# Kernel tuning notes

Hardware: AMD Instinct MI355X
Metric: run time of the kernel (lower is better)

## Reference

```python
import jax, jax.numpy as jnp
import numpy as np

EMBED_DIM = 1024
NUM_HEADS = 16
HEAD_DIM = EMBED_DIM // NUM_HEADS
TOPK_INIT = 0.3  # learnable scalar in torch; k = int(S*sigmoid(topk)) is non-differentiable, so static here


def setup_inputs() -> dict:
    rng = jax.random.key(0)
    ks = jax.random.split(rng, 11)
    L, N, E = 2048, 2, EMBED_DIM
    S = 2048
    w = 1.0 / np.sqrt(E)
    return {
        "query": jax.random.normal(ks[0], (L, N, E), jnp.float32),
        "key": jax.random.normal(ks[1], (S, N, E), jnp.float32),
        "value": jax.random.normal(ks[2], (S, N, E), jnp.float32),
        "Wq": jax.random.normal(ks[3], (E, E), jnp.float32) * w,
        "bq": jax.random.normal(ks[4], (E,), jnp.float32) * 0.02,
        "Wk": jax.random.normal(ks[5], (E, E), jnp.float32) * w,
        "bk": jax.random.normal(ks[6], (E,), jnp.float32) * 0.02,
        "Wv": jax.random.normal(ks[7], (E, E), jnp.float32) * w,
        "bv": jax.random.normal(ks[8], (E,), jnp.float32) * 0.02,
        "Wo": jax.random.normal(ks[9], (E, E), jnp.float32) * w,
        "bo": jax.random.normal(ks[10], (E,), jnp.float32) * 0.02,
    }


def reference(query, key, value, Wq, bq, Wk, bk, Wv, bv, Wo, bo):
    L, N, E = query.shape
    S = key.shape[0]
    H, D = NUM_HEADS, HEAD_DIM

    # Linear projections (nn.Linear: y = x @ W.T + b), then [L/S,N,E] -> [N,L/S,H,D]
    q = (query @ Wq.T + bq).reshape(L, N, H, D).transpose(1, 0, 2, 3)
    k = (key @ Wk.T + bk).reshape(S, N, H, D).transpose(1, 0, 2, 3)
    v = (value @ Wv.T + bv).reshape(S, N, H, D).transpose(1, 0, 2, 3)

    # [N, L, H, S]
    scores = jnp.einsum('nlhd,nshd->nlhs', q, k) / np.sqrt(D).astype(np.float32)

    # per-query top-k sparsification; k is static (int() of sigmoid(param) in torch)
    k_sel = int(S * (1.0 / (1.0 + np.exp(-TOPK_INIT))))
    _, topk_idx = jax.lax.top_k(scores, k_sel)
    keep = jnp.put_along_axis(
        jnp.zeros(scores.shape, dtype=bool), topk_idx, True, axis=-1, inplace=False
    )
    scores = jnp.where(keep, scores, -jnp.inf)
    attn = jax.nn.softmax(scores, axis=-1)

    # [N, L, D, H] (note d-major, h-minor ordering matches torch's view(L,N,E))
    out = jnp.einsum('nlhs,nshd->nldh', attn, v)
    out = out.transpose(1, 0, 2, 3).reshape(L, N, E)
    return out @ Wo.T + bo
```

## Files before the change

### kernel.cpp

```cpp
#include <hip/hip_runtime.h>
#include <hip/hip_bf16.h>
#include <hip/hip_fp16.h>


#define KSEL 1176u
#define SROW 2048
#define HSTR 132

typedef __attribute__((ext_vector_type(8))) short bf16x8;
typedef __attribute__((ext_vector_type(8))) _Float16 f16x8;
typedef __attribute__((ext_vector_type(4))) float f32x4;
typedef unsigned short ushort_t;

union S8 { bf16x8 v; ushort_t u[8]; };
union H8 { f16x8 v; ushort_t u[8]; };

#define MFMA16(A, B, C)  __builtin_amdgcn_mfma_f32_16x16x32_bf16(A, B, C, 0, 0, 0)
#define MFMAH16(A, B, C) __builtin_amdgcn_mfma_f32_16x16x32_f16(A, B, C, 0, 0, 0)

__device__ __forceinline__ ushort_t f2bf(float x) {
  unsigned u = __float_as_uint(x);
  return (ushort_t)((u + 0x7FFFu + ((u >> 16) & 1u)) >> 16);
}
__device__ __forceinline__ float bf2f(ushort_t b) {
  return __uint_as_float(((unsigned)b) << 16);
}
__device__ __forceinline__ ushort_t f2h(float x) {
  return __half_as_ushort(__float2half(x));
}
__device__ __forceinline__ float h2f(ushort_t b) {
  return __half2float(__ushort_as_half(b));
}

__device__ __forceinline__ void cvt8(ushort_t* dst, float4 p, float4 q) {
  H8 t;
  t.u[0] = f2h(p.x); t.u[1] = f2h(p.y); t.u[2] = f2h(p.z); t.u[3] = f2h(p.w);
  t.u[4] = f2h(q.x); t.u[5] = f2h(q.y); t.u[6] = f2h(q.z); t.u[7] = f2h(q.w);
  *(f16x8*)dst = t.v;
}

__global__ __launch_bounds__(256) void presplit_w(
    const float* __restrict__ W0, const float* __restrict__ W1,
    const float* __restrict__ W2, const float* __restrict__ W3,
    ushort_t* __restrict__ Whi, ushort_t* __restrict__ Wlo) {
  const int m = blockIdx.y;
  const float* W = (m == 0) ? W0 : (m == 1) ? W1 : (m == 2) ? W2 : W3;
  const size_t off = ((size_t)blockIdx.x * 256 + threadIdx.x) * 8;
  const size_t base = (size_t)m * 1048576 + off;
  if (m == 3) {
    const int f = (int)(off >> 10);
    const int r = (int)(off & 1023);
    const int hcol = r >> 6, d0 = r & 63;
    S8 hi_, lo_;
#pragma unroll
    for (int j = 0; j < 8; j++) {
      float x = W[(size_t)f * 1024 + (size_t)(d0 + j) * 16 + hcol];
      ushort_t hb = f2bf(x);
      hi_.u[j] = hb;
      lo_.u[j] = f2bf(x - bf2f(hb));
    }
    *(bf16x8*)&Whi[base] = hi_.v;
    *(bf16x8*)&Wlo[base] = lo_.v;
  } else {
    float4 p = *(const float4*)&W[off];
    float4 q = *(const float4*)&W[off + 4];
    cvt8(&Whi[base], p, q);
  }
}

__global__ __launch_bounds__(256, 4) void proj_qkv(
    const float* __restrict__ Xq, const float* __restrict__ Xk,
    const float* __restrict__ Xv, const float* __restrict__ bq,
    const float* __restrict__ bk, const float* __restrict__ bv,
    const ushort_t* __restrict__ Whi, ushort_t* __restrict__ Qf,
    ushort_t* __restrict__ Kf, ushort_t* __restrict__ Vt) {
  __shared__ ushort_t Ah[64 * 72], Bh[64 * 72];
  const int z = blockIdx.z;
  const float* X = (z == 0) ? Xq : (z == 1) ? Xk : Xv;
  const float* bias = (z == 0) ? bq : (z == 1) ? bk : bv;
  const size_t zoff = (size_t)z * 1048576;

  const int tid = threadIdx.x;
  const int n0 = blockIdx.x * 64, m0 = blockIdx.y * 64;
  const int lane = tid & 63, wv = tid >> 6;
  const int lg = lane >> 4, lq = lane & 15;
  const int wr = wv >> 1, wc = wv & 1;
  const int sr = tid >> 2, c8 = (tid & 3) * 8;

  f32x4 acc[2][2] = {};

  const float* Xr = &X[(size_t)(m0 + sr) * 1024 + c8];
  const ushort_t* Bhg = Whi + zoff + (size_t)(n0 + sr) * 1024 + c8;

  float4 a0 = *(const float4*)&Xr[0],  a1 = *(const float4*)&Xr[4];
  float4 a2 = *(const float4*)&Xr[32], a3 = *(const float4*)&Xr[36];
  f16x8 pb0 = *(const f16x8*)&Bhg[0], pb1 = *(const f16x8*)&Bhg[32];

  for (int k0 = 0; k0 < 1024; k0 += 64) {
    __syncthreads();
    cvt8(&Ah[sr * 72 + c8], a0, a1);
    cvt8(&Ah[sr * 72 + c8 + 32], a2, a3);
    *(f16x8*)&Bh[sr * 72 + c8] = pb0;
    *(f16x8*)&Bh[sr * 72 + c8 + 32] = pb1;
    if (k0 + 64 < 1024) {
      const float* Xn = Xr + k0 + 64;
      a0 = *(const float4*)&Xn[0];  a1 = *(const float4*)&Xn[4];
      a2 = *(const float4*)&Xn[32]; a3 = *(const float4*)&Xn[36];
      pb0 = *(const f16x8*)&Bhg[k0 + 64];
      pb1 = *(const f16x8*)&Bhg[k0 + 96];
    }
    __syncthreads();
#pragma unroll
    for (int kh = 0; kh < 2; kh++) {
      const int ko = kh * 32 + lg * 8;
      f16x8 bh0 = *(const f16x8*)&Bh[(wc * 32 + lq) * 72 + ko];
      f16x8 bh1 = *(const f16x8*)&Bh[(wc * 32 + 16 + lq) * 72 + ko];
#pragma unroll
      for (int i = 0; i < 2; i++) {
        f16x8 ahv = *(const f16x8*)&Ah[(wr * 32 + i * 16 + lq) * 72 + ko];
        acc[i][0] = MFMAH16(ahv, bh0, acc[i][0]);
        acc[i][1] = MFMAH16(ahv, bh1, acc[i][1]);
      }
    }
  }

  ushort_t* dqk = (z == 0) ? Qf : Kf;
#pragma unroll
  for (int i = 0; i < 2; i++)
#pragma unroll
    for (int j = 0; j < 2; j++)
#pragma unroll
      for (int ri = 0; ri < 4; ri++) {
        int m = m0 + wr * 32 + i * 16 + 4 * lg + ri;
        int e = n0 + wc * 32 + j * 16 + lq;
        float v = acc[i][j][ri] + bias[e];
        int l = m >> 1, n = m & 1, hh = e >> 6, d = e & 63;
        if (z == 2) {
          Vt[((size_t)(n * 16 + hh) * 64 + d) * 2048 + l] = f2h(v);
        } else {
          float x = (z == 0) ? v * 0.125f : v;
          dqk[((size_t)(n * 16 + hh) * 2048 + l) * 64 + d] = f2h(x);
        }
      }
}

__global__ __launch_bounds__(256, 4) void proj_out(
    const ushort_t* __restrict__ AOhi, const ushort_t* __restrict__ AOlo,
    const ushort_t* __restrict__ Whi3, const ushort_t* __restrict__ Wlo3,
    const float* __restrict__ bias, float* __restrict__ out) {
  __shared__ ushort_t Ah[64 * 72], Al[64 * 72], Bh[64 * 72], Bl[64 * 72];
  const int tid = threadIdx.x;
  const int n0 = blockIdx.x * 64, m0 = blockIdx.y * 64;
  const int lane = tid & 63, wv = tid >> 6;
  const int lg = lane >> 4, lq = lane & 15;
  const int wr = wv >> 1, wc = wv & 1;
  const int sr = tid >> 2, c8 = (tid & 3) * 8;

  f32x4 acc[2][2] = {};

  const size_t abase = (size_t)(m0 + sr) * 64 + c8;
  const ushort_t* Bhg = Whi3 + (size_t)(n0 + sr) * 1024 + c8;
  const ushort_t* Blg = Wlo3 + (size_t)(n0 + sr) * 1024 + c8;

  bf16x8 pa0 = *(const bf16x8*)&AOhi[abase], pa1 = *(const bf16x8*)&AOhi[abase + 32];
  bf16x8 pc0 = *(const bf16x8*)&AOlo[abase], pc1 = *(const bf16x8*)&AOlo[abase + 32];
  bf16x8 pb0 = *(const bf16x8*)&Bhg[0], pb1 = *(const bf16x8*)&Bhg[32];
  bf16x8 pl0 = *(const bf16x8*)&Blg[0], pl1 = *(const bf16x8*)&Blg[32];

  for (int k0 = 0; k0 < 1024; k0 += 64) {
    __syncthreads();
    *(bf16x8*)&Ah[sr * 72 + c8] = pa0;  *(bf16x8*)&Ah[sr * 72 + c8 + 32] = pa1;
    *(bf16x8*)&Al[sr * 72 + c8] = pc0;  *(bf16x8*)&Al[sr * 72 + c8 + 32] = pc1;
    *(bf16x8*)&Bh[sr * 72 + c8] = pb0;  *(bf16x8*)&Bh[sr * 72 + c8 + 32] = pb1;
    *(bf16x8*)&Bl[sr * 72 + c8] = pl0;  *(bf16x8*)&Bl[sr * 72 + c8 + 32] = pl1;
    if (k0 + 64 < 1024) {
      const size_t an = abase + (size_t)((k0 >> 6) + 1) * 262144;
      pa0 = *(const bf16x8*)&AOhi[an]; pa1 = *(const bf16x8*)&AOhi[an + 32];
      pc0 = *(const bf16x8*)&AOlo[an]; pc1 = *(const bf16x8*)&AOlo[an + 32];
      pb0 = *(const bf16x8*)&Bhg[k0 + 64]; pb1 = *(const bf16x8*)&Bhg[k0 + 96];
      pl0 = *(const bf16x8*)&Blg[k0 + 64]; pl1 = *(const bf16x8*)&Blg[k0 + 96];
    }
    __syncthreads();
#pragma unroll
    for (int kh = 0; kh < 2; kh++) {
      const int ko = kh * 32 + lg * 8;
      bf16x8 bh0 = *(const bf16x8*)&Bh[(wc * 32 + lq) * 72 + ko];
      bf16x8 bh1 = *(const bf16x8*)&Bh[(wc * 32 + 16 + lq) * 72 + ko];
      bf16x8 bl0 = *(const bf16x8*)&Bl[(wc * 32 + lq) * 72 + ko];
      bf16x8 bl1 = *(const bf16x8*)&Bl[(wc * 32 + 16 + lq) * 72 + ko];
#pragma unroll
      for (int i = 0; i < 2; i++) {
        bf16x8 ahv = *(const bf16x8*)&Ah[(wr * 32 + i * 16 + lq) * 72 + ko];
        bf16x8 alv = *(const bf16x8*)&Al[(wr * 32 + i * 16 + lq) * 72 + ko];
        acc[i][0] = MFMA16(ahv, bh0, acc[i][0]);
        acc[i][0] = MFMA16(alv, bh0, acc[i][0]);
        acc[i][0] = MFMA16(ahv, bl0, acc[i][0]);
        acc[i][1] = MFMA16(ahv, bh1, acc[i][1]);
        acc[i][1] = MFMA16(alv, bh1, acc[i][1]);
        acc[i][1] = MFMA16(ahv, bl1, acc[i][1]);
      }
    }
  }

#pragma unroll
  for (int i = 0; i < 2; i++)
#pragma unroll
    for (int j = 0; j < 2; j++)
#pragma unroll
      for (int ri = 0; ri < 4; ri++) {
        int m = m0 + wr * 32 + i * 16 + 4 * lg + ri;
        int e = n0 + wc * 32 + j * 16 + lq;
        out[(size_t)m * 1024 + e] = acc[i][j][ri] + bias[e];
      }
}

template <bool RANKMAP>
__device__ __forceinline__ void scan_row(const unsigned* hrow, unsigned target,
                                         int lane, int* binOut, unsigned* remOut) {
  unsigned c0, c1, c2, c3;
  if (RANKMAP) {
    const bool neg = lane >= 32;
    const int ho = neg ? (lane << 1) : (62 - (lane << 1));
    uint2 hw = *(const uint2*)&hrow[ho];
    unsigned a0 = hw.x & 0xffffu, a1 = hw.x >> 16;
    unsigned a2 = hw.y & 0xffffu, a3 = hw.y >> 16;
    c0 = neg ? a0 : a3; c1 = neg ? a1 : a2;
    c2 = neg ? a2 : a1; c3 = neg ? a3 : a0;
  } else {
    uint2 hw = *(const uint2*)&hrow[lane << 1];
    c0 = hw.x & 0xffffu; c1 = hw.x >> 16;
    c2 = hw.y & 0xffffu; c3 = hw.y >> 16;
  }
  unsigned s4 = c0 + c1 + c2 + c3, incl = s4;
#pragma unroll
  for (int off = 1; off < 64; off <<= 1) {
    unsigned t = __shfl_up(incl, off);
    if (lane >= off) incl += t;
  }
  unsigned excl = incl - s4;
  bool found = (excl < target) && (target <= incl);
  int b = 0; unsigned rm = 1;
  if (found) {
    unsigned cum = excl;
    if (cum + c0 >= target) { b = (lane << 2); rm = target - cum; }
    else { cum += c0;
      if (cum + c1 >= target) { b = (lane << 2) + 1; rm = target - cum; }
      else { cum += c1;
        if (cum + c2 >= target) { b = (lane << 2) + 2; rm = target - cum; }
        else { cum += c2; b = (lane << 2) + 3; rm = target - cum; } } }
  }
  unsigned long long bal = __ballot(found);
  int src = (int)__builtin_ctzll(bal);
  *binOut = __shfl(b, src);
  *remOut = (unsigned)__shfl((int)rm, src);
}

#define KLOAD(F, gg)                                                   \
  do {                                                                 \
    _Pragma("unroll") for (int tt = 0; tt < 4; tt++) {                 \
      const int koff = ((gg) * 4 + tt) * 1024;                         \
      F[tt * 2 + 0] = *(const f16x8*)&kbase[koff];                     \
      F[tt * 2 + 1] = *(const f16x8*)&kbase[koff + 32];                \
    }                                                                  \
  } while (0)

#define KCOMP(F, gg)                                                          \
  do {                                                                        \
    _Pragma("unroll") for (int tt = 0; tt < 4; tt++) {                        \
      f32x4 acc_ = {0.f, 0.f, 0.f, 0.f};                                      \
      acc_ = MFMAH16(F[tt * 2 + 0], qf0, acc_);                               \
      acc_ = MFMAH16(F[tt * 2 + 1], qf1, acc_);                               \
      uint2 pw_;                                                              \
      pw_.x = (unsigned)f2h(acc_[0]) | ((unsigned)f2h(acc_[1]) << 16);        \
      pw_.y = (unsigned)f2h(acc_[2]) | ((unsigned)f2h(acc_[3]) << 16);        \
      atomicAdd(&histP[lq * HSTR + ((pw_.x >> 9) & 0x7Fu)],                   \
                1u << (((pw_.x >> 8) & 1u) << 4));                            \
      atomicAdd(&histP[lq * HSTR + (pw_.x >> 25)],                            \
                1u << (((pw_.x >> 24) & 1u) << 4));                           \
      atomicAdd(&histP[lq * HSTR + ((pw_.y >> 9) & 0x7Fu)],                   \
                1u << (((pw_.y >> 8) & 1u) << 4));                            \
      atomicAdd(&histP[lq * HSTR + (pw_.y >> 25)],                            \
                1u << (((pw_.y >> 24) & 1u) << 4));                           \
      const int st_ = (w * 16 + (gg) * 4 + tt) * 16;                          \
      *(uint2*)&scH[lq * SROW + ((st_ + 4 * lg) ^ xr8q)] = pw_;               \
    }                                                                         \
  } while (0)

__global__ __launch_bounds__(512, 2) void sparse_attn(
    const ushort_t* __restrict__ Qf, const ushort_t* __restrict__ Kfp,
    const ushort_t* __restrict__ Vt, ushort_t* __restrict__ AOhi,
    ushort_t* __restrict__ AOlo) {
  __shared__ ushort_t scH[16 * SROW];
  __shared__ unsigned histP[16 * HSTR];
  __shared__ float Obuf[16 * 68];
  __shared__ float dinvS[16];

  const int flat = blockIdx.x + 128 * (blockIdx.y + 16 * blockIdx.z);
  const int idx = (flat & 7) * 512 + (flat >> 3);
  const int lb = idx & 127, h = (idx >> 7) & 15, n = idx >> 11;

  const int tid = threadIdx.x;
  const int lane = tid & 63, w = tid >> 6;
  const int lg = lane >> 4, lq = lane & 15;
  const int xr8q = (lq & 7) << 3;
  const size_t nh = (size_t)(n * 16 + h);

  for (int i = tid; i < 16 * HSTR; i += 512) histP[i] = 0u;
  for (int i = tid; i < 16 * 68; i += 512) Obuf[i] = 0.f;

  const size_t qo = (nh * 2048 + (size_t)lb * 16 + lq) * 64 + lg * 8;
  const f16x8 qf0 = *(const f16x8*)&Qf[qo];
  const f16x8 qf1 = *(const f16x8*)&Qf[qo + 32];

  const ushort_t* Kf = Kfp + nh * 2048 * 64;
  const ushort_t* kbase = Kf + (size_t)(w * 256 + lq) * 64 + lg * 8;

  __syncthreads();

  {
    f16x8 fa[8], fb[8];
    KLOAD(fa, 0);
    for (int g = 0; g < 4; g += 2) {
      KLOAD(fb, g + 1);
      KCOMP(fa, g);
      if (g + 2 < 4) KLOAD(fa, g + 2);
      KCOMP(fb, g + 1);
    }
  }
  __syncthreads();

  for (int rr = 0; rr < 2; rr++) {
    const int r = w * 2 + rr;
    const int rb = r * SROW;
    const int xr = (r & 7) << 3;
    unsigned* hrow = &histP[r * HSTR];

    int b1r; unsigned rem;
    scan_row<true>(hrow, KSEL, lane, &b1r, &rem);
    const unsigned rb1 = (b1r < 128) ? (unsigned)(b1r ^ 0x7F) : (unsigned)b1r;
    const unsigned sxor = (rb1 & 0x80u) ? 0u : 0xFFu;

    uint4 rv0 = *(const uint4*)&scH[rb + ((0 * 512 + lane * 8) ^ xr)];
    uint4 rv1 = *(const uint4*)&scH[rb + ((1 * 512 + lane * 8) ^ xr)];
    uint4 rv2 = *(const uint4*)&scH[rb + ((2 * 512 + lane * 8) ^ xr)];
    uint4 rv3 = *(const uint4*)&scH[rb + ((3 * 512 + lane * 8) ^ xr)];

    *(uint2*)&hrow[lane << 1] = make_uint2(0u, 0u);
    __threadfence_block();
    auto refine1 = [&](unsigned wd) {
      if (((wd >> 8) & 0xFFu) == rb1) {
        unsigned sr_ = (wd & 0xFFu) ^ sxor;
        atomicAdd(&hrow[sr_ >> 1], 1u << ((sr_ & 1u) << 4));
      }
      if ((wd >> 24) == rb1) {
        unsigned sr_ = ((wd >> 16) & 0xFFu) ^ sxor;
        atomicAdd(&hrow[sr_ >> 1], 1u << ((sr_ & 1u) << 4));
      }
    };
    refine1(rv0.x); refine1(rv0.y); refine1(rv0.z); refine1(rv0.w);
    refine1(rv1.x); refine1(rv1.y); refine1(rv1.z); refine1(rv1.w);
    refine1(rv2.x); refine1(rv2.y); refine1(rv2.z); refine1(rv2.w);
    refine1(rv3.x); refine1(rv3.y); refine1(rv3.z); refine1(rv3.w);
    __threadfence_block();
    int b2r; unsigned rem2;
    scan_row<false>(hrow, rem, lane, &b2r, &rem2);
    const unsigned vbits = (rb1 << 8) | (((unsigned)b2r) ^ sxor);
    const float fV = h2f((ushort_t)vbits);

    float den = 0.f;
    auto exp2w = [&](unsigned wd) -> unsigned {
      float f0 = h2f((ushort_t)(wd & 0xffffu));
      float f1 = h2f((ushort_t)(wd >> 16));
      float e0 = (f0 >= fV) ? __expf(f0) : 0.f;
      float e1 = (f1 >= fV) ? __expf(f1) : 0.f;
      den += e0 + e1;
      return (unsigned)f2h(e0) | ((unsigned)f2h(e1) << 16);
    };
    uint4 ov;
    ov.x = exp2w(rv0.x); ov.y = exp2w(rv0.y); ov.z = exp2w(rv0.z); ov.w = exp2w(rv0.w);
    *(uint4*)&scH[rb + ((0 * 512 + lane * 8) ^ xr)] = ov;
    ov.x = exp2w(rv1.x); ov.y = exp2w(rv1.y); ov.z = exp2w(rv1.z); ov.w = exp2w(rv1.w);
    *(uint4*)&scH[rb + ((1 * 512 + lane * 8) ^ xr)] = ov;
    ov.x = exp2w(rv2.x); ov.y = exp2w(rv2.y); ov.z = exp2w(rv2.z); ov.w = exp2w(rv2.w);
    *(uint4*)&scH[rb + ((2 * 512 + lane * 8) ^ xr)] = ov;
    ov.x = exp2w(rv3.x); ov.y = exp2w(rv3.y); ov.z = exp2w(rv3.z); ov.w = exp2w(rv3.w);
    *(uint4*)&scH[rb + ((3 * 512 + lane * 8) ^ xr)] = ov;

#pragma unroll
    for (int off = 32; off > 0; off >>= 1) den += __shfl_xor(den, off);
    if (lane == 0) dinvS[r] = 1.0f / den;
  }
  __syncthreads();

  {
    const int db = w & 3, sh = w >> 2;
    const int sOff = sh * 1024;
    const ushort_t* Vb =
        Vt + (nh * 64 + (size_t)(db * 16 + lq)) * 2048 + sOff;
    const int xw = (lq & 7) << 3;
    const int arow = lq * SROW;
    f32x4 o0 = {0.f, 0.f, 0.f, 0.f}, o1 = o0, o2 = o0, o3 = o0;
    f16x8 va0 = *(const f16x8*)&Vb[lg * 8];
    f16x8 va1 = *(const f16x8*)&Vb[32 + lg * 8];
    f16x8 vb0 = *(const f16x8*)&Vb[64 + lg * 8];
    f16x8 vb1 = *(const f16x8*)&Vb[96 + lg * 8];
#pragma unroll 2
    for (int c = 0; c < 16; c += 2) {
      f16x8 na0, na1, nb0, nb1;
      if (c + 2 < 16) {
        na0 = *(const f16x8*)&Vb[(c + 2) * 64 + lg * 8];
        na1 = *(const f16x8*)&Vb[(c + 2) * 64 + 32 + lg * 8];
        nb0 = *(const f16x8*)&Vb[(c + 3) * 64 + lg * 8];
        nb1 = *(const f16x8*)&Vb[(c + 3) * 64 + 32 + lg * 8];
      }
      f16x8 pa0 = *(const f16x8*)&scH[arow + ((sOff + c * 64 + lg * 8) ^ xw)];
      f16x8 pa1 = *(const f16x8*)&scH[arow + ((sOff + c * 64 + 32 + lg * 8) ^ xw)];
      o0 = MFMAH16(pa0, va0, o0);
      o1 = MFMAH16(pa1, va1, o1);
      f16x8 pb0_ = *(const f16x8*)&scH[arow + ((sOff + (c + 1) * 64 + lg * 8) ^ xw)];
      f16x8 pb1_ = *(const f16x8*)&scH[arow + ((sOff + (c + 1) * 64 + 32 + lg * 8) ^ xw)];
      o2 = MFMAH16(pb0_, vb0, o2);
      o3 = MFMAH16(pb1_, vb1, o3);
      va0 = na0; va1 = na1; vb0 = nb0; vb1 = nb1;
    }
    f32x4 oa = (o0 + o1) + (o2 + o3);
#pragma unroll
    for (int ri = 0; ri < 4; ri++) {
      int q = lg * 4 + ri;
      atomicAdd(&Obuf[q * 68 + db * 16 + lq], oa[ri]);
    }
  }
  __syncthreads();

  {
#pragma unroll
    for (int rep = 0; rep < 2; rep++) {
      int idx2 = tid + rep * 512;
      int q = idx2 >> 6, d = idx2 & 63;
      float val = Obuf[q * 68 + d] * dinvS[q];
      size_t ai = ((size_t)h * 4096 + (size_t)(lb * 16 + q) * 2 + n) * 64 +
                  (size_t)d;
      ushort_t hb = f2bf(val);
      AOhi[ai] = hb;
      AOlo[ai] = f2bf(val - bf2f(hb));
    }
  }
}

extern "C" void kernel_launch(void* const* d_in, const int* in_sizes, int n_in,
                              void* d_out, int out_size, void* d_ws, size_t ws_size,
                              hipStream_t stream) {
  const float* query = (const float*)d_in[0];
  const float* key   = (const float*)d_in[1];
  const float* value = (const float*)d_in[2];
  const float* Wq    = (const float*)d_in[3];
  const float* bq    = (const float*)d_in[4];
  const float* Wk    = (const float*)d_in[5];
  const float* bk    = (const float*)d_in[6];
  const float* Wv    = (const float*)d_in[7];
  const float* bv    = (const float*)d_in[8];
  const float* Wo    = (const float*)d_in[9];
  const float* bo    = (const float*)d_in[10];

  ushort_t* Qf   = (ushort_t*)d_ws;
  ushort_t* Kf   = Qf + 4194304;
  ushort_t* Vt   = Kf + 4194304;
  ushort_t* AOhi = Vt + 4194304;
  ushort_t* AOlo = AOhi + 4194304;
  ushort_t* Whi  = AOlo + 4194304;
  ushort_t* Wlo  = Whi + 4194304;

  dim3 block(256);
  presplit_w<<<dim3(512, 4), block, 0, stream>>>(Wq, Wk, Wv, Wo, Whi, Wlo);

  proj_qkv<<<dim3(16, 64, 3), block, 0, stream>>>(query, key, value, bq, bk, bv,
                                                  Whi, Qf, Kf, Vt);

  sparse_attn<<<dim3(128, 16, 2), dim3(512), 0, stream>>>(Qf, Kf, Vt, AOhi, AOlo);

  proj_out<<<dim3(16, 64), block, 0, stream>>>(AOhi, AOlo, Whi + 3 * 1048576,
                                               Wlo + 3 * 1048576, bo,
                                               (float*)d_out);
}
```

Baseline: 363.2 us.

## Fuse exp/threshold into PV MFMA loop and fold log2e into Q scale

```diff
diff --git a/kernel.cpp b/kernel.cpp
--- a/kernel.cpp
+++ b/kernel.cpp
@@ -138,7 +138,7 @@
         if (z == 2) {
           Vt[((size_t)(n * 16 + hh) * 64 + d) * 2048 + l] = f2h(v);
         } else {
-          float x = (z == 0) ? v * 0.125f : v;
+          float x = (z == 0) ? v * (0.125f * 1.4426950408889634f) : v;
           dqk[((size_t)(n * 16 + hh) * 2048 + l) * 64 + d] = f2h(x);
         }
       }
@@ -293,6 +293,8 @@
   __shared__ ushort_t scH[16 * SROW];
   __shared__ unsigned histP[16 * HSTR];
   __shared__ float Obuf[16 * 68];
+  __shared__ float denS[16];
+  __shared__ float fVS[16];
   __shared__ float dinvS[16];
 
   const int flat = blockIdx.x + 128 * (blockIdx.y + 16 * blockIdx.z);
@@ -307,6 +309,7 @@
 
   for (int i = tid; i < 16 * HSTR; i += 512) histP[i] = 0u;
   for (int i = tid; i < 16 * 68; i += 512) Obuf[i] = 0.f;
+  if (tid < 16) denS[tid] = 0.f;
 
   const size_t qo = (nh * 2048 + (size_t)lb * 16 + lq) * 64 + lg * 8;
   const f16x8 qf0 = *(const f16x8*)&Qf[qo];
@@ -364,72 +367,64 @@
     __threadfence_block();
     int b2r; unsigned rem2;
     scan_row<false>(hrow, rem, lane, &b2r, &rem2);
+    (void)rem2;
     const unsigned vbits = (rb1 << 8) | (((unsigned)b2r) ^ sxor);
-    const float fV = h2f((ushort_t)vbits);
-
-    float den = 0.f;
-    auto exp2w = [&](unsigned wd) -> unsigned {
-      float f0 = h2f((ushort_t)(wd & 0xffffu));
-      float f1 = h2f((ushort_t)(wd >> 16));
-      float e0 = (f0 >= fV) ? __expf(f0) : 0.f;
-      float e1 = (f1 >= fV) ? __expf(f1) : 0.f;
-      den += e0 + e1;
-      return (unsigned)f2h(e0) | ((unsigned)f2h(e1) << 16);
-    };
-    uint4 ov;
-    ov.x = exp2w(rv0.x); ov.y = exp2w(rv0.y); ov.z = exp2w(rv0.z); ov.w = exp2w(rv0.w);
-    *(uint4*)&scH[rb + ((0 * 512 + lane * 8) ^ xr)] = ov;
-    ov.x = exp2w(rv1.x); ov.y = exp2w(rv1.y); ov.z = exp2w(rv1.z); ov.w = exp2w(rv1.w);
-    *(uint4*)&scH[rb + ((1 * 512 + lane * 8) ^ xr)] = ov;
-    ov.x = exp2w(rv2.x); ov.y = exp2w(rv2.y); ov.z = exp2w(rv2.z); ov.w = exp2w(rv2.w);
-    *(uint4*)&scH[rb + ((2 * 512 + lane * 8) ^ xr)] = ov;
-    ov.x = exp2w(rv3.x); ov.y = exp2w(rv3.y); ov.z = exp2w(rv3.z); ov.w = exp2w(rv3.w);
-    *(uint4*)&scH[rb + ((3 * 512 + lane * 8) ^ xr)] = ov;
-
-#pragma unroll
-    for (int off = 32; off > 0; off >>= 1) den += __shfl_xor(den, off);
-    if (lane == 0) dinvS[r] = 1.0f / den;
+    if (lane == 0) fVS[r] = h2f((ushort_t)vbits);
   }
   __syncthreads();
 
   {
-    const int db = w & 3, sh = w >> 2;
-    const int sOff = sh * 1024;
-    const ushort_t* Vb =
-        Vt + (nh * 64 + (size_t)(db * 16 + lq)) * 2048 + sOff;
-    const int xw = (lq & 7) << 3;
+    const int sOff = w * 256;
+    const int xr = (lq & 7) << 3;
     const int arow = lq * SROW;
+    const float fV = fVS[lq];
+    const ushort_t* Vb = Vt + (nh * 64 + (size_t)lq) * 2048 + sOff + lg * 8;
     f32x4 o0 = {0.f, 0.f, 0.f, 0.f}, o1 = o0, o2 = o0, o3 = o0;
-    f16x8 va0 = *(const f16x8*)&Vb[lg * 8];
-    f16x8 va1 = *(const f16x8*)&Vb[32 + lg * 8];
-    f16x8 vb0 = *(const f16x8*)&Vb[64 + lg * 8];
-    f16x8 vb1 = *(const f16x8*)&Vb[96 + lg * 8];
-#pragma unroll 2
-    for (int c = 0; c < 16; c += 2) {
-      f16x8 na0, na1, nb0, nb1;
-      if (c + 2 < 16) {
-        na0 = *(const f16x8*)&Vb[(c + 2) * 64 + lg * 8];
-        na1 = *(const f16x8*)&Vb[(c + 2) * 64 + 32 + lg * 8];
-        nb0 = *(const f16x8*)&Vb[(c + 3) * 64 + lg * 8];
-        nb1 = *(const f16x8*)&Vb[(c + 3) * 64 + 32 + lg * 8];
-      }
-      f16x8 pa0 = *(const f16x8*)&scH[arow + ((sOff + c * 64 + lg * 8) ^ xw)];
-      f16x8 pa1 = *(const f16x8*)&scH[arow + ((sOff + c * 64 + 32 + lg * 8) ^ xw)];
-      o0 = MFMAH16(pa0, va0, o0);
-      o1 = MFMAH16(pa1, va1, o1);
-      f16x8 pb0_ = *(const f16x8*)&scH[arow + ((sOff + (c + 1) * 64 + lg * 8) ^ xw)];
-      f16x8 pb1_ = *(const f16x8*)&scH[arow + ((sOff + (c + 1) * 64 + 32 + lg * 8) ^ xw)];
-      o2 = MFMAH16(pb0_, vb0, o2);
-      o3 = MFMAH16(pb1_, vb1, o3);
-      va0 = na0; va1 = na1; vb0 = nb0; vb1 = nb1;
-    }
-    f32x4 oa = (o0 + o1) + (o2 + o3);
+    float den0 = 0.f, den1 = 0.f;
+    f16x8 v0 = *(const f16x8*)&Vb[0];
+    f16x8 v1 = *(const f16x8*)&Vb[16 * 2048];
+    f16x8 v2 = *(const f16x8*)&Vb[32 * 2048];
+    f16x8 v3 = *(const f16x8*)&Vb[48 * 2048];
+    f16x8 sa = *(const f16x8*)&scH[arow + ((sOff + lg * 8) ^ xr)];
+#pragma unroll
+    for (int ks = 0; ks < 8; ks++) {
+      f16x8 nv0, nv1, nv2, nv3, nsa;
+      if (ks + 1 < 8) {
+        const int ko = (ks + 1) * 32;
+        nv0 = *(const f16x8*)&Vb[ko];
+        nv1 = *(const f16x8*)&Vb[ko + 16 * 2048];
+        nv2 = *(const f16x8*)&Vb[ko + 32 * 2048];
+        nv3 = *(const f16x8*)&Vb[ko + 48 * 2048];
+        nsa = *(const f16x8*)&scH[arow + ((sOff + ko + lg * 8) ^ xr)];
+      }
+      H8 su; su.v = sa;
+      H8 pu;
+#pragma unroll
+      for (int j = 0; j < 8; j += 2) {
+        float f0 = h2f(su.u[j]), f1 = h2f(su.u[j + 1]);
+        float e0 = (f0 >= fV) ? __builtin_amdgcn_exp2f(f0) : 0.f;
+        float e1 = (f1 >= fV) ? __builtin_amdgcn_exp2f(f1) : 0.f;
+        den0 += e0; den1 += e1;
+        pu.u[j] = f2h(e0); pu.u[j + 1] = f2h(e1);
+      }
+      o0 = MFMAH16(pu.v, v0, o0);
+      o1 = MFMAH16(pu.v, v1, o1);
+      o2 = MFMAH16(pu.v, v2, o2);
+      o3 = MFMAH16(pu.v, v3, o3);
+      v0 = nv0; v1 = nv1; v2 = nv2; v3 = nv3; sa = nsa;
+    }
+    atomicAdd(&denS[lq], den0 + den1);
 #pragma unroll
     for (int ri = 0; ri < 4; ri++) {
-      int q = lg * 4 + ri;
-      atomicAdd(&Obuf[q * 68 + db * 16 + lq], oa[ri]);
-    }
-  }
+      const int qrow = lg * 4 + ri;
+      atomicAdd(&Obuf[qrow * 68 + lq], o0[ri]);
+      atomicAdd(&Obuf[qrow * 68 + 16 + lq], o1[ri]);
+      atomicAdd(&Obuf[qrow * 68 + 32 + lq], o2[ri]);
+      atomicAdd(&Obuf[qrow * 68 + 48 + lq], o3[ri]);
+    }
+  }
+  __syncthreads();
+  if (tid < 16) dinvS[tid] = 1.0f / denS[tid];
   __syncthreads();
 
   {
```

Measured after the change: 481.0 us. 32.5% more time.
